# Optimization experiments

Hardware: AMD Instinct MI355X
Metric: run time of the kernel (lower is better)

## Reference

```python
import jax, jax.numpy as jnp
import numpy as np

# Dims: T=out_seq_len, B=batch, D=hidden_dim, H=hidden_dim_de, E=embedding_size, C=feat_channels
T, B, D, H, E, C, FH, FW = 32, 16, 512, 512, 512, 512, 8, 32


def _lstm_dir(x_seq, W_ih, W_hh, b_ih, b_hh, reverse):
    # x_seq: (T, B, D); PyTorch gate order i, f, g, o
    gx = jnp.einsum('tbd,gd->tbg', x_seq, W_ih) + b_ih  # (T, B, 4H)
    Hh = W_hh.shape[1]
    def step(carry, g_t):
        h, c = carry
        g = g_t + h @ W_hh.T + b_hh
        i, f, gg, o = jnp.split(g, 4, axis=-1)
        c = jax.nn.sigmoid(f) * c + jax.nn.sigmoid(i) * jnp.tanh(gg)
        h = jax.nn.sigmoid(o) * jnp.tanh(c)
        return (h, c), h
    init = (jnp.zeros((x_seq.shape[1], Hh), x_seq.dtype),
            jnp.zeros((x_seq.shape[1], Hh), x_seq.dtype))
    _, hs = jax.lax.scan(step, init, gx, reverse=reverse)
    return hs  # (T, B, H)


def setup_inputs() -> dict:
    key = jax.random.key(0)
    ks = jax.random.split(key, 16)
    s = 0.02
    inp = {
        'hidden_en': jax.random.normal(ks[0], (T, B, D), jnp.float32),
        'conv_f': jax.random.normal(ks[1], (B, C, FH, FW), jnp.float32),
        # bidirectional LSTM params (PyTorch layout: W_ih (4H, D), W_hh (4H, H))
        'W_ih_f': jax.random.normal(ks[2], (4 * H, D), jnp.float32) * s,
        'W_hh_f': jax.random.normal(ks[3], (4 * H, H), jnp.float32) * s,
        'b_ih_f': jnp.zeros((4 * H,), jnp.float32),
        'b_hh_f': jnp.zeros((4 * H,), jnp.float32),
        'W_ih_b': jax.random.normal(ks[4], (4 * H, D), jnp.float32) * s,
        'W_hh_b': jax.random.normal(ks[5], (4 * H, H), jnp.float32) * s,
        'b_ih_b': jnp.zeros((4 * H,), jnp.float32),
        'b_hh_b': jnp.zeros((4 * H,), jnp.float32),
        # linear_decode: (H, 2H)
        'W_dec': jax.random.normal(ks[6], (H, 2 * H), jnp.float32) * s,
        'b_dec': jnp.zeros((H,), jnp.float32),
        # conv_em: 3x3, C -> E (OIHW)
        'W_em': jax.random.normal(ks[7], (E, C, 3, 3), jnp.float32) * s,
        'b_em': jnp.zeros((E,), jnp.float32),
        # attention h_em: 1x1 conv == linear H -> E
        'W_hem': jax.random.normal(ks[8], (E, H), jnp.float32) * s,
        'b_hem': jnp.zeros((E,), jnp.float32),
        # conv_att: 1x1 conv E -> 1
        'w_att': jax.random.normal(ks[9], (E,), jnp.float32) * s,
        'b_att': jnp.zeros((), jnp.float32),
    }
    return inp


def reference(hidden_en, conv_f, W_ih_f, W_hh_f, b_ih_f, b_hh_f,
              W_ih_b, W_hh_b, b_ih_b, b_hh_b, W_dec, b_dec,
              W_em, b_em, W_hem, b_hem, w_att, b_att):
    # decoder_ctc: bidirectional LSTM + linear
    h_fwd = _lstm_dir(hidden_en, W_ih_f, W_hh_f, b_ih_f, b_hh_f, reverse=False)
    h_bwd = _lstm_dir(hidden_en, W_ih_b, W_hh_b, b_ih_b, b_hh_b, reverse=True)
    hidden_de = jnp.concatenate([h_fwd, h_bwd], axis=-1) @ W_dec.T + b_dec  # (T, B, H)

    # conv_em: 3x3 same-padding conv, NCHW
    x_em = jax.lax.conv_general_dilated(
        conv_f, W_em, window_strides=(1, 1), padding='SAME',
        dimension_numbers=('NCHW', 'OIHW', 'NCHW')) + b_em[None, :, None, None]  # (B,E,FH,FW)
    att_x_em = jnp.transpose(x_em.reshape(x_em.shape[0], E, -1), (0, 2, 1))  # (B, HW, E)

    # batched attention over all timesteps (dropout is identity at eval)
    h_em = jnp.einsum('tbh,eh->tbe', hidden_de, W_hem) + b_hem  # (T, B, E)
    feat = jnp.tanh(x_em[None] + h_em[:, :, :, None, None])     # (T, B, E, FH, FW)
    scores = jnp.einsum('tbehw,e->tbhw', feat, w_att) + b_att   # (T, B, FH, FW)
    alpha = jax.nn.softmax(scores.reshape(scores.shape[0], scores.shape[1], -1), axis=-1)  # (T,B,HW)
    att = jnp.einsum('tbn,bne->tbe', alpha, att_x_em)           # (T, B, E)

    ctc_out = jnp.concatenate([hidden_de, att], axis=-1)        # (T, B, H+E)
    return jnp.transpose(ctc_out, (1, 0, 2))                    # (B, T, H+E)
```

## Files before the change

### kernel.cpp

```cpp
#include <hip/hip_runtime.h>
#include <hip/hip_bf16.h>
#include <math.h>

#define T_LEN 32
#define BATCH 16
#define DDIM  512
#define HDIM  512
#define EDIM  512
#define CDIM  512
#define FHH   8
#define FWW   32
#define HW    256
#define G4    2048
#define PADH  10
#define PADW  34
#define WLP   520

typedef __attribute__((ext_vector_type(8))) short bf16x8;
typedef __attribute__((ext_vector_type(4))) float f32x4;

__device__ __forceinline__ ushort bfr(float x) {
    union { float f; uint32_t u; } c; c.f = x;
    uint32_t r = (c.u + 0x7FFFu + ((c.u >> 16) & 1u)) >> 16;
    return (ushort)r;
}

__device__ __forceinline__ float frcp(float x) { return __builtin_amdgcn_rcpf(x); }
__device__ __forceinline__ float ftanh(float x) {
    return 1.f - 2.f * frcp(1.f + __expf(2.f * x));
}
__device__ __forceinline__ float fsig(float x) {
    return frcp(1.f + __expf(-x));
}

__device__ __forceinline__ void ld_lds16(const void* g, void* l) {
    __builtin_amdgcn_global_load_lds((const __attribute__((address_space(1))) void*)g,
                                     (__attribute__((address_space(3))) void*)l, 16, 0, 0);
}

__device__ __forceinline__ void st_u16_sc1(ushort* p, ushort v) {
    asm volatile("global_store_short %0, %1, off sc1" :: "v"(p), "v"((uint)v) : "memory");
}
__device__ __forceinline__ void st_i32_sc1(int* p, int v) {
    asm volatile("global_store_dword %0, %1, off sc1" :: "v"(p), "v"(v) : "memory");
}
__device__ __forceinline__ void st_f32_sc1(float* p, float v) {
    asm volatile("global_store_dword %0, %1, off sc1" :: "v"(p), "v"(v) : "memory");
}
__device__ __forceinline__ int ld_i32_sc1(const int* p) {
    int v;
    asm volatile("global_load_dword %0, %1, off sc1\n\ts_waitcnt vmcnt(0)"
                 : "=v"(v) : "v"(p) : "memory");
    return v;
}

struct PrepArgs { const float* s[7]; ushort* d[7]; };
__global__ __launch_bounds__(256) void prep_all(
    PrepArgs a, int* __restrict__ syncbuf,
    const float* __restrict__ conv_f, ushort* __restrict__ padT,
    const float* __restrict__ W_em, ushort* __restrict__ Wt)
{
    __shared__ float tile[32][33];
    const int bid = blockIdx.x, tid = threadIdx.x;
    if (bid < 5120) {
        int i = bid * 256 + tid;
        if (i < 80) st_i32_sc1(syncbuf + i, 0);
        const int e0 = 65536, e1 = 327680, e2 = 589824, e3 = 851968,
                  e4 = 1114112, e5 = 1245184;
        int seg, base;
        if      (i < e0) { seg = 0; base = 0;  }
        else if (i < e1) { seg = 1; base = e0; }
        else if (i < e2) { seg = 2; base = e1; }
        else if (i < e3) { seg = 3; base = e2; }
        else if (i < e4) { seg = 4; base = e3; }
        else if (i < e5) { seg = 5; base = e4; }
        else             { seg = 6; base = e5; }
        int li = i - base;
        float4 v = ((const float4*)a.s[seg])[li];
        ushort4 o;
        o.x = bfr(v.x); o.y = bfr(v.y); o.z = bfr(v.z); o.w = bfr(v.w);
        ((ushort4*)a.d[seg])[li] = o;
        return;
    }
    if (bid < 7168) {
        int id = bid - 5120;
        int s0 = (id & 7) * 32, c0 = ((id >> 3) & 15) * 32, b = id >> 7;
        int lo = tid & 31, hi = tid >> 5;
#pragma unroll
        for (int it = 0; it < 4; ++it) {
            int cl = hi + it * 8;
            tile[cl][lo] = conv_f[((size_t)(b * CDIM + c0 + cl)) * HW + s0 + lo];
        }
        __syncthreads();
#pragma unroll
        for (int it = 0; it < 4; ++it) {
            int sl = hi + it * 8;
            int s = s0 + sl;
            int y = s >> 5, x = s & 31;
            padT[(((size_t)b * PADH + y + 1) * PADW + (x + 1)) * CDIM + c0 + lo] =
                bfr(tile[lo][sl]);
        }
        return;
    }
    if (bid < 7840) {
        int gid = (bid - 7168) * 256 + tid;
        int c4 = gid & 127;
        int cellb = gid >> 7;
        int cell = cellb % 84;
        int b = cellb / 84;
        int y, x;
        if (cell < 34) { y = 0; x = cell; }
        else if (cell < 68) { y = 9; x = cell - 34; }
        else { int k2 = cell - 68; y = 1 + (k2 >> 1); x = (k2 & 1) ? 33 : 0; }
        ((ushort4*)padT)[(((size_t)b * PADH + y) * PADW + x) * (CDIM / 4) + c4] =
            make_ushort4(0, 0, 0, 0);
        return;
    }
    {
        int gid = (bid - 7840) * 256 + tid;
        int c = gid % CDIM;
        int t = gid / CDIM;
        int e = t % EDIM;
        int tap = t / EDIM;
        int dy = tap / 3, dx = tap % 3;
        Wt[gid] = bfr(W_em[((e * CDIM + c) * 3 + dy) * 3 + dx]);
    }
}

__device__ __forceinline__ void tile64_compute(
    const ushort* Ap0, const ushort* Bp0, int K,
    ushort* smem, int tid, f32x4 (&acc)[2][2])
{
    ushort* As = smem;
    ushort* Bs = smem + 2048;
    const int w = tid >> 6, lane = tid & 63;
    ushort* AsW = &As[w * 512];
    ushort* BsW = &Bs[w * 512];
    const int wm = (w >> 1) * 32, wn = (w & 1) * 32;
    const int kb = (lane >> 4) * 8, fr = lane & 15;
    for (int kk = 0; kk < K; kk += 32) {
        __syncthreads();
        ld_lds16(Ap0 + kk, AsW);
        ld_lds16(Bp0 + kk, BsW);
        __syncthreads();
        bf16x8 af[2], bg[2];
#pragma unroll
        for (int i = 0; i < 2; ++i)
            af[i] = *(const bf16x8*)&As[(wm + i * 16 + fr) * 32 + kb];
#pragma unroll
        for (int j = 0; j < 2; ++j)
            bg[j] = *(const bf16x8*)&Bs[(wn + j * 16 + fr) * 32 + kb];
#pragma unroll
        for (int i = 0; i < 2; ++i)
#pragma unroll
            for (int j = 0; j < 2; ++j)
                acc[i][j] = __builtin_amdgcn_mfma_f32_16x16x32_bf16(af[i], bg[j], acc[i][j], 0, 0, 0);
    }
}

__global__ __launch_bounds__(256) void gemm64(
    const ushort* __restrict__ A, const ushort* __restrict__ B,
    const float* __restrict__ bias0,
    float* __restrict__ C, ushort* __restrict__ Cbf, float* __restrict__ Cscat,
    int M, int N, int K)
{
    __shared__ ushort smem[4096];
    const int n0 = blockIdx.x * 64, m0 = blockIdx.y * 64;
    const int tid = threadIdx.x, w = tid >> 6, lane = tid & 63;
    const int r0 = tid >> 2, c0 = (tid & 3) * 8;
    f32x4 acc[2][2];
#pragma unroll
    for (int i = 0; i < 2; ++i)
#pragma unroll
        for (int j = 0; j < 2; ++j) acc[i][j] = {0.f, 0.f, 0.f, 0.f};
    tile64_compute(A + (size_t)(m0 + r0) * K + c0, B + (size_t)(n0 + r0) * K + c0,
                   K, smem, tid, acc);
    const int wm = (w >> 1) * 32, wn = (w & 1) * 32;
    const int col = lane & 15, rq = (lane >> 4) * 4;
#pragma unroll
    for (int i = 0; i < 2; ++i) {
#pragma unroll
        for (int r = 0; r < 4; ++r) {
            int m = m0 + wm + i * 16 + rq + r;
#pragma unroll
            for (int j = 0; j < 2; ++j) {
                int n = n0 + wn + j * 16 + col;
                float v = acc[i][j][r];
                if (bias0) v += bias0[n];
                if (C)   C[(size_t)m * N + n] = v;
                if (Cbf) Cbf[(size_t)m * N + n] = bfr(v);
                if (Cscat) {
                    int t = m >> 4, b = m & 15;
                    Cscat[((size_t)(b * T_LEN + t)) * 1024 + n] = v;
                }
            }
        }
    }
}

__global__ __launch_bounds__(256) void fused_main(
    const ushort* __restrict__ Whh_f, const ushort* __restrict__ Whh_b,
    float* __restrict__ gx_f, float* __restrict__ gx_b,
    const ushort* __restrict__ hen_bf,
    const ushort* __restrict__ Wih_f, const ushort* __restrict__ Wih_b,
    const float* __restrict__ b_ih_f, const float* __restrict__ b_hh_f,
    const float* __restrict__ b_ih_b, const float* __restrict__ b_hh_b,
    ushort* __restrict__ hs_bf,
    int* __restrict__ syncbuf,
    const ushort* __restrict__ padT, const ushort* __restrict__ Wt,
    const float* __restrict__ bias_em, float* __restrict__ xem)
{
    __shared__ ushort smem[64 * WLP];
    const int bid = blockIdx.x, tid = threadIdx.x;
    const int w = tid >> 6, lane = tid & 63;
    int* flags = syncbuf;
    int* gcnt  = syncbuf + 64;

    if (bid < 64) {
        const int dir = bid >> 5;
        const int j0 = (bid & 31) * 16;
        const ushort* W = dir ? Whh_b : Whh_f;
        const float* gx = dir ? gx_b : gx_f;
#pragma unroll
        for (int i = 0; i < 16; ++i) {
            int row = w * 16 + i;
            int g = row >> 4, jl = row & 15;
            bf16x8 v = *(const bf16x8*)(W + ((size_t)(g * 512 + j0 + jl)) * 512 + lane * 8);
            *(bf16x8*)&smem[row * WLP + lane * 8] = v;
        }
        __syncthreads();
        if (tid >= 64) return;
        __builtin_amdgcn_s_setprio(1);

        const int fr = lane & 15, kq = lane >> 4;
        const int j = j0 + fr;
        const int* fq = &flags[dir * 32 + (lane & 31)];
        f32x4 cr = {0.f, 0.f, 0.f, 0.f};
        int mt_done = -1;
        for (int step = 0; step < T_LEN; ++step) {
            const int tcur = dir ? (T_LEN - 1 - step) : step;
            const int mt = tcur >> 2;
            if (mt != mt_done) {
                const int* gp = &gcnt[dir * 8 + mt];
                for (;;) {
                    int v = ld_i32_sc1(gp);
                    if (v >= 32) break;
                    __builtin_amdgcn_s_sleep(4);
                }
                mt_done = mt;
            }
            float gxv[4][4];
#pragma unroll
            for (int r = 0; r < 4; ++r) {
                const float* gxr = gx + ((size_t)tcur * BATCH + (kq * 4 + r)) * G4 + j;
#pragma unroll
                for (int g = 0; g < 4; ++g)
                    asm volatile("global_load_dword %0, %1, off sc1"
                                 : "=v"(gxv[r][g]) : "v"(gxr + g * 512));
            }
            f32x4 acc[4];
#pragma unroll
            for (int g = 0; g < 4; ++g) acc[g] = {0.f, 0.f, 0.f, 0.f};
            if (step > 0) {
                const int tprev = dir ? tcur + 1 : tcur - 1;
                const ushort* hp = hs_bf + ((size_t)tprev * BATCH + fr) * 1024 + dir * 512 + kq * 8;
                bf16x8 hreg[16];
#pragma unroll
                for (int u = 0; u < 16; ++u)
                    asm volatile("global_load_dwordx4 %0, %1, off sc1"
                                 : "=v"(hreg[u]) : "v"(hp + u * 32));
                asm volatile("s_waitcnt vmcnt(0)" ::: "memory");
                __builtin_amdgcn_sched_barrier(0);
#pragma unroll
                for (int u = 0; u < 16; ++u) {
#pragma unroll
                    for (int g = 0; g < 4; ++g) {
                        bf16x8 bb = *(const bf16x8*)&smem[(g * 16 + fr) * WLP + kq * 8 + u * 32];
                        acc[g] = __builtin_amdgcn_mfma_f32_16x16x32_bf16(hreg[u], bb, acc[g], 0, 0, 0);
                    }
                }
            } else {
                asm volatile("s_waitcnt vmcnt(0)" ::: "memory");
                __builtin_amdgcn_sched_barrier(0);
            }
#pragma unroll
            for (int r = 0; r < 4; ++r) {
                int b = kq * 4 + r;
                float gi = gxv[r][0] + acc[0][r];
                float gf = gxv[r][1] + acc[1][r];
                float gg = gxv[r][2] + acc[2][r];
                float go = gxv[r][3] + acc[3][r];
                float si = fsig(gi), sf = fsig(gf), so = fsig(go);
                float c = sf * cr[r] + si * ftanh(gg);
                cr[r] = c;
                float h = so * ftanh(c);
                st_u16_sc1(hs_bf + ((size_t)tcur * BATCH + b) * 1024 + dir * 512 + j, bfr(h));
            }
            if (step < T_LEN - 1) {
                asm volatile("s_waitcnt vmcnt(0)" ::: "memory");
                if (lane == 0) st_i32_sc1(&flags[bid], step + 1);
                const int need = step + 1;
                for (;;) {
                    int v = ld_i32_sc1(fq);
                    if (__all(v >= need)) break;
                    __builtin_amdgcn_s_sleep(1);
                }
            }
        }
        return;
    }

    if (bid < 576) {
        const int gi = bid - 64;
        const int dir = gi & 1;
        const int q = gi >> 1;
        const int nt = q & 31;
        const int mt0 = q >> 5;
        const int mtile = dir ? (7 - mt0) : mt0;
        const ushort* Bw = dir ? Wih_b : Wih_f;
        const float* bi0 = dir ? b_ih_b : b_ih_f;
        const float* bi1 = dir ? b_hh_b : b_hh_f;
        float* Cg = dir ? gx_b : gx_f;
        const int m0 = mtile * 64, n0 = nt * 64;
        const int r0 = tid >> 2, c0 = (tid & 3) * 8;
        f32x4 acc[2][2];
#pragma unroll
        for (int i = 0; i < 2; ++i)
#pragma unroll
            for (int j = 0; j < 2; ++j) acc[i][j] = {0.f, 0.f, 0.f, 0.f};
        tile64_compute(hen_bf + (size_t)(m0 + r0) * 512 + c0,
                       Bw + (size_t)(n0 + r0) * 512 + c0, 512, smem, tid, acc);
        const int wm = (w >> 1) * 32, wn = (w & 1) * 32;
        const int col = lane & 15, rq = (lane >> 4) * 4;
#pragma unroll
        for (int i = 0; i < 2; ++i)
#pragma unroll
            for (int r = 0; r < 4; ++r) {
                int m = m0 + wm + i * 16 + rq + r;
#pragma unroll
                for (int j2 = 0; j2 < 2; ++j2) {
                    int n = n0 + wn + j2 * 16 + col;
                    st_f32_sc1(&Cg[(size_t)m * G4 + n], acc[i][j2][r] + bi0[n] + bi1[n]);
                }
            }
        asm volatile("s_waitcnt vmcnt(0)" ::: "memory");
        __syncthreads();
        if (tid == 0) atomicAdd(&gcnt[dir * 8 + mtile], 1);
        return;
    }

    {
        const int cbid = bid - 576;
        const int n0 = (cbid & 7) * 64, m0 = (cbid >> 3) * 64;
        const int r0 = tid >> 2, c0 = (tid & 3) * 8;
        const int b = m0 >> 8, s0 = m0 & 255, y0 = s0 >> 5;
        const int y = y0 + (r0 >> 5), x = r0 & 31;
        const ushort* Abase = padT + (((size_t)b * PADH + y) * PADW + x) * CDIM + c0;
        const ushort* Bbase = Wt + (size_t)(n0 + r0) * CDIM + c0;
        f32x4 acc[2][2];
#pragma unroll
        for (int i = 0; i < 2; ++i)
#pragma unroll
            for (int j = 0; j < 2; ++j) acc[i][j] = {0.f, 0.f, 0.f, 0.f};
        for (int tap = 0; tap < 9; ++tap) {
            const int dy = tap / 3, dx = tap % 3;
            tile64_compute(Abase + ((size_t)dy * PADW + dx) * CDIM,
                           Bbase + (size_t)tap * EDIM * CDIM, 512, smem, tid, acc);
        }
        const int wm = (w >> 1) * 32, wn = (w & 1) * 32;
        const int col = lane & 15, rq = (lane >> 4) * 4;
#pragma unroll
        for (int i = 0; i < 2; ++i)
#pragma unroll
            for (int r = 0; r < 4; ++r) {
                int m = m0 + wm + i * 16 + rq + r;
                int s = m & 255;
#pragma unroll
                for (int j2 = 0; j2 < 2; ++j2) {
                    int e = n0 + wn + j2 * 16 + col;
                    xem[((size_t)b * EDIM + e) * HW + s] = acc[i][j2][r] + bias_em[e];
                }
            }
    }
}

__global__ __launch_bounds__(256) void attention(
    const float* __restrict__ xem,
    const float* __restrict__ hem,
    const float* __restrict__ watt,
    float* __restrict__ out) {
    int i = blockIdx.x;
    int k = i >> 3;
    int b = ((i & 7) << 1) | (k & 1);
    int t = k >> 1;
    int tb = t * 16 + b;
    int tid = threadIdx.x;
    __shared__ float hl[512], wl[512], al[256], red[8];
    for (int q = tid; q < 512; q += 256) { hl[q] = hem[(size_t)tb * 512 + q]; wl[q] = watt[q]; }
    __syncthreads();
    const float* xb = xem + (size_t)b * EDIM * HW;
    float sc = 0.f;
#pragma unroll 4
    for (int e = 0; e < 512; ++e)
        sc += ftanh(xb[(size_t)e * HW + tid] + hl[e]) * wl[e];
    float m = sc;
#pragma unroll
    for (int o = 32; o; o >>= 1) m = fmaxf(m, __shfl_xor(m, o));
    if ((tid & 63) == 0) red[tid >> 6] = m;
    __syncthreads();
    m = fmaxf(fmaxf(red[0], red[1]), fmaxf(red[2], red[3]));
    float ex = __expf(sc - m);
    float s = ex;
#pragma unroll
    for (int o = 32; o; o >>= 1) s += __shfl_xor(s, o);
    if ((tid & 63) == 0) red[4 + (tid >> 6)] = s;
    __syncthreads();
    s = red[4] + red[5] + red[6] + red[7];
    al[tid] = ex * frcp(s);
    __syncthreads();
    float* ob = out + ((size_t)(b * T_LEN + t)) * 1024 + 512;
    for (int eo = 0; eo < 512; eo += 256) {
        int e = eo + tid;
        const float* xr = xb + (size_t)e * HW;
        float acc = 0.f;
#pragma unroll 4
        for (int n = 0; n < 256; n += 4) {
            float4 v = *(const float4*)&xr[n];
            acc += al[n] * v.x + al[n + 1] * v.y + al[n + 2] * v.z + al[n + 3] * v.w;
        }
        ob[e] = acc;
    }
}

extern "C" void kernel_launch(void* const* d_in, const int* in_sizes, int n_in,
                              void* d_out, int out_size, void* d_ws, size_t ws_size,
                              hipStream_t stream) {
    const float* hidden_en = (const float*)d_in[0];
    const float* conv_f    = (const float*)d_in[1];
    const float* W_ih_f    = (const float*)d_in[2];
    const float* W_hh_f    = (const float*)d_in[3];
    const float* b_ih_f    = (const float*)d_in[4];
    const float* b_hh_f    = (const float*)d_in[5];
    const float* W_ih_b    = (const float*)d_in[6];
    const float* W_hh_b    = (const float*)d_in[7];
    const float* b_ih_b    = (const float*)d_in[8];
    const float* b_hh_b    = (const float*)d_in[9];
    const float* W_dec     = (const float*)d_in[10];
    const float* b_dec     = (const float*)d_in[11];
    const float* W_em      = (const float*)d_in[12];
    const float* b_em      = (const float*)d_in[13];
    const float* W_hem     = (const float*)d_in[14];
    const float* b_hem     = (const float*)d_in[15];
    const float* w_att     = (const float*)d_in[16];
    float* out = (float*)d_out;

    char* p = (char*)d_ws;
    auto alloc = [&](size_t bytes) { void* r = p; p += (bytes + 255) & ~(size_t)255; return r; };
    float*    gx_f    = (float*)alloc((size_t)T_LEN * BATCH * G4 * 4);
    float*    gx_b    = (float*)alloc((size_t)T_LEN * BATCH * G4 * 4);
    float*    h_em    = (float*)alloc((size_t)T_LEN * BATCH * 512 * 4);
    float*    x_em    = (float*)alloc((size_t)BATCH * EDIM * HW * 4);
    ushort*   padT    = (ushort*)alloc((size_t)BATCH * PADH * PADW * CDIM * 2);
    ushort*   Wt      = (ushort*)alloc((size_t)9 * EDIM * CDIM * 2);
    ushort*   hen_bf  = (ushort*)alloc((size_t)T_LEN * BATCH * DDIM * 2);
    ushort*   Wihf_bf = (ushort*)alloc((size_t)G4 * DDIM * 2);
    ushort*   Wihb_bf = (ushort*)alloc((size_t)G4 * DDIM * 2);
    ushort*   Whhf_bf = (ushort*)alloc((size_t)G4 * HDIM * 2);
    ushort*   Whhb_bf = (ushort*)alloc((size_t)G4 * HDIM * 2);
    ushort*   Wdec_bf = (ushort*)alloc((size_t)HDIM * 1024 * 2);
    ushort*   Whem_bf = (ushort*)alloc((size_t)EDIM * HDIM * 2);
    ushort*   hs_bf   = (ushort*)alloc((size_t)T_LEN * BATCH * 1024 * 2);
    ushort*   hde_bf  = (ushort*)alloc((size_t)T_LEN * BATCH * 512 * 2);
    int*      syncbuf = (int*)alloc(512);

    PrepArgs pa;
    pa.s[0] = hidden_en; pa.d[0] = hen_bf;
    pa.s[1] = W_ih_f;    pa.d[1] = Wihf_bf;
    pa.s[2] = W_ih_b;    pa.d[2] = Wihb_bf;
    pa.s[3] = W_hh_f;    pa.d[3] = Whhf_bf;
    pa.s[4] = W_hh_b;    pa.d[4] = Whhb_bf;
    pa.s[5] = W_dec;     pa.d[5] = Wdec_bf;
    pa.s[6] = W_hem;     pa.d[6] = Whem_bf;
    prep_all<<<17056, 256, 0, stream>>>(pa, syncbuf, conv_f, padT, W_em, Wt);

    fused_main<<<1088, 256, 0, stream>>>(Whhf_bf, Whhb_bf, gx_f, gx_b, hen_bf,
                                         Wihf_bf, Wihb_bf, b_ih_f, b_hh_f,
                                         b_ih_b, b_hh_b, hs_bf, syncbuf,
                                         padT, Wt, b_em, x_em);

    gemm64<<<dim3(8, 8), 256, 0, stream>>>(hs_bf, Wdec_bf, b_dec,
                                           nullptr, hde_bf, out, 512, 512, 1024);

    gemm64<<<dim3(8, 8), 256, 0, stream>>>(hde_bf, Whem_bf, b_hem,
                                           h_em, nullptr, nullptr, 512, 512, 512);

    attention<<<512, 256, 0, stream>>>(x_em, h_em, w_att, out);
}
```

Baseline: 253.1 us.

## Fold decode and h_em weights, split LSTM into separate persistent kernel

Precomputes a combined weight W_hem·W_dec and a combined bias so h_em is computed straight from the LSTM hidden states, which removes the serial decode→h_em GEMM dependency. The attention and both output GEMMs move into one tail kernel that synchronises per tile through counters. The conv, input-projection and weight-combination GEMMs run in a worker kernel ahead of the LSTM, so the LSTM no longer waits on flags or overlaps with them. The gx buffer is interleaved by gate so each LSTM step needs one float4 load per row. In exchange, the LSTM recurrence can no longer overlap with the conv GEMM, there is an extra launch, and the combined weight is rounded to bf16 once more.

```diff
diff --git a/kernel.cpp b/kernel.cpp
--- a/kernel.cpp
+++ b/kernel.cpp
@@ -53,12 +53,21 @@
                  : "=v"(v) : "v"(p) : "memory");
     return v;
 }
+__device__ __forceinline__ float ld_f32_sc1(const float* p) {
+    float v;
+    asm volatile("global_load_dword %0, %1, off sc1\n\ts_waitcnt vmcnt(0)"
+                 : "=v"(v) : "v"(p) : "memory");
+    return v;
+}
 
 struct PrepArgs { const float* s[7]; ushort* d[7]; };
 __global__ __launch_bounds__(256) void prep_all(
     PrepArgs a, int* __restrict__ syncbuf,
     const float* __restrict__ conv_f, ushort* __restrict__ padT,
-    const float* __restrict__ W_em, ushort* __restrict__ Wt)
+    const float* __restrict__ W_em, ushort* __restrict__ Wt,
+    const float* __restrict__ W_dec, ushort* __restrict__ WdecT,
+    const float* __restrict__ W_hem, const float* __restrict__ b_dec,
+    const float* __restrict__ b_hem, float* __restrict__ b_comb)
 {
     __shared__ float tile[32][33];
     const int bid = blockIdx.x, tid = threadIdx.x;
@@ -116,7 +125,7 @@
             make_ushort4(0, 0, 0, 0);
         return;
     }
-    {
+    if (bid < 17056) {
         int gid = (bid - 7840) * 256 + tid;
         int c = gid % CDIM;
         int t = gid / CDIM;
@@ -124,6 +133,32 @@
         int tap = t / EDIM;
         int dy = tap / 3, dx = tap % 3;
         Wt[gid] = bfr(W_em[((e * CDIM + c) * 3 + dy) * 3 + dx]);
+        return;
+    }
+    if (bid < 17568) {
+        int idx = bid - 17056;
+        int ht = idx & 15, kt = idx >> 4;
+        int h0 = ht * 32, k0 = kt * 32;
+        int lo = tid & 31, hi = tid >> 5;
+#pragma unroll
+        for (int it = 0; it < 4; ++it) {
+            int i = hi + it * 8;
+            tile[i][lo] = W_dec[(size_t)(h0 + i) * 1024 + k0 + lo];
+        }
+        __syncthreads();
+#pragma unroll
+        for (int it = 0; it < 4; ++it) {
+            int i = hi + it * 8;
+            WdecT[(size_t)(k0 + i) * 512 + h0 + lo] = bfr(tile[lo][i]);
+        }
+        return;
+    }
+    {
+        int e = (bid - 17568) * 256 + tid;
+        float s = b_hem[e];
+        const float* wr = W_hem + (size_t)e * 512;
+        for (int h = 0; h < 512; ++h) s += wr[h] * b_dec[h];
+        b_comb[e] = s;
     }
 }
 
@@ -158,217 +193,40 @@
     }
 }
 
-__global__ __launch_bounds__(256) void gemm64(
-    const ushort* __restrict__ A, const ushort* __restrict__ B,
-    const float* __restrict__ bias0,
-    float* __restrict__ C, ushort* __restrict__ Cbf, float* __restrict__ Cscat,
-    int M, int N, int K)
-{
-    __shared__ ushort smem[4096];
-    const int n0 = blockIdx.x * 64, m0 = blockIdx.y * 64;
-    const int tid = threadIdx.x, w = tid >> 6, lane = tid & 63;
-    const int r0 = tid >> 2, c0 = (tid & 3) * 8;
-    f32x4 acc[2][2];
-#pragma unroll
-    for (int i = 0; i < 2; ++i)
-#pragma unroll
-        for (int j = 0; j < 2; ++j) acc[i][j] = {0.f, 0.f, 0.f, 0.f};
-    tile64_compute(A + (size_t)(m0 + r0) * K + c0, B + (size_t)(n0 + r0) * K + c0,
-                   K, smem, tid, acc);
-    const int wm = (w >> 1) * 32, wn = (w & 1) * 32;
-    const int col = lane & 15, rq = (lane >> 4) * 4;
-#pragma unroll
-    for (int i = 0; i < 2; ++i) {
-#pragma unroll
-        for (int r = 0; r < 4; ++r) {
-            int m = m0 + wm + i * 16 + rq + r;
-#pragma unroll
-            for (int j = 0; j < 2; ++j) {
-                int n = n0 + wn + j * 16 + col;
-                float v = acc[i][j][r];
-                if (bias0) v += bias0[n];
-                if (C)   C[(size_t)m * N + n] = v;
-                if (Cbf) Cbf[(size_t)m * N + n] = bfr(v);
-                if (Cscat) {
-                    int t = m >> 4, b = m & 15;
-                    Cscat[((size_t)(b * T_LEN + t)) * 1024 + n] = v;
-                }
-            }
-        }
-    }
-}
-
-__global__ __launch_bounds__(256) void fused_main(
-    const ushort* __restrict__ Whh_f, const ushort* __restrict__ Whh_b,
-    float* __restrict__ gx_f, float* __restrict__ gx_b,
+__global__ __launch_bounds__(256) void workers(
+    const ushort* __restrict__ padT, const ushort* __restrict__ Wt,
+    const float* __restrict__ bias_em, float* __restrict__ xem,
     const ushort* __restrict__ hen_bf,
     const ushort* __restrict__ Wih_f, const ushort* __restrict__ Wih_b,
     const float* __restrict__ b_ih_f, const float* __restrict__ b_hh_f,
     const float* __restrict__ b_ih_b, const float* __restrict__ b_hh_b,
-    ushort* __restrict__ hs_bf,
-    int* __restrict__ syncbuf,
-    const ushort* __restrict__ padT, const ushort* __restrict__ Wt,
-    const float* __restrict__ bias_em, float* __restrict__ xem)
+    float* __restrict__ gxT_f, float* __restrict__ gxT_b,
+    const ushort* __restrict__ Whem_bf, const ushort* __restrict__ WdecT_bf,
+    ushort* __restrict__ Wcomb_bf)
 {
-    __shared__ ushort smem[64 * WLP];
+    __shared__ ushort smem[4096];
     const int bid = blockIdx.x, tid = threadIdx.x;
     const int w = tid >> 6, lane = tid & 63;
-    int* flags = syncbuf;
-    int* gcnt  = syncbuf + 64;
-
-    if (bid < 64) {
-        const int dir = bid >> 5;
-        const int j0 = (bid & 31) * 16;
-        const ushort* W = dir ? Whh_b : Whh_f;
-        const float* gx = dir ? gx_b : gx_f;
-#pragma unroll
-        for (int i = 0; i < 16; ++i) {
-            int row = w * 16 + i;
-            int g = row >> 4, jl = row & 15;
-            bf16x8 v = *(const bf16x8*)(W + ((size_t)(g * 512 + j0 + jl)) * 512 + lane * 8);
-            *(bf16x8*)&smem[row * WLP + lane * 8] = v;
-        }
-        __syncthreads();
-        if (tid >= 64) return;
-        __builtin_amdgcn_s_setprio(1);
-
-        const int fr = lane & 15, kq = lane >> 4;
-        const int j = j0 + fr;
-        const int* fq = &flags[dir * 32 + (lane & 31)];
-        f32x4 cr = {0.f, 0.f, 0.f, 0.f};
-        int mt_done = -1;
-        for (int step = 0; step < T_LEN; ++step) {
-            const int tcur = dir ? (T_LEN - 1 - step) : step;
-            const int mt = tcur >> 2;
-            if (mt != mt_done) {
-                const int* gp = &gcnt[dir * 8 + mt];
-                for (;;) {
-                    int v = ld_i32_sc1(gp);
-                    if (v >= 32) break;
-                    __builtin_amdgcn_s_sleep(4);
-                }
-                mt_done = mt;
-            }
-            float gxv[4][4];
-#pragma unroll
-            for (int r = 0; r < 4; ++r) {
-                const float* gxr = gx + ((size_t)tcur * BATCH + (kq * 4 + r)) * G4 + j;
-#pragma unroll
-                for (int g = 0; g < 4; ++g)
-                    asm volatile("global_load_dword %0, %1, off sc1"
-                                 : "=v"(gxv[r][g]) : "v"(gxr + g * 512));
-            }
-            f32x4 acc[4];
-#pragma unroll
-            for (int g = 0; g < 4; ++g) acc[g] = {0.f, 0.f, 0.f, 0.f};
-            if (step > 0) {
-                const int tprev = dir ? tcur + 1 : tcur - 1;
-                const ushort* hp = hs_bf + ((size_t)tprev * BATCH + fr) * 1024 + dir * 512 + kq * 8;
-                bf16x8 hreg[16];
-#pragma unroll
-                for (int u = 0; u < 16; ++u)
-                    asm volatile("global_load_dwordx4 %0, %1, off sc1"
-                                 : "=v"(hreg[u]) : "v"(hp + u * 32));
-                asm volatile("s_waitcnt vmcnt(0)" ::: "memory");
-                __builtin_amdgcn_sched_barrier(0);
-#pragma unroll
-                for (int u = 0; u < 16; ++u) {
-#pragma unroll
-                    for (int g = 0; g < 4; ++g) {
-                        bf16x8 bb = *(const bf16x8*)&smem[(g * 16 + fr) * WLP + kq * 8 + u * 32];
-                        acc[g] = __builtin_amdgcn_mfma_f32_16x16x32_bf16(hreg[u], bb, acc[g], 0, 0, 0);
-                    }
-                }
-            } else {
-                asm volatile("s_waitcnt vmcnt(0)" ::: "memory");
-                __builtin_amdgcn_sched_barrier(0);
-            }
-#pragma unroll
-            for (int r = 0; r < 4; ++r) {
-                int b = kq * 4 + r;
-                float gi = gxv[r][0] + acc[0][r];
-                float gf = gxv[r][1] + acc[1][r];
-                float gg = gxv[r][2] + acc[2][r];
-                float go = gxv[r][3] + acc[3][r];
-                float si = fsig(gi), sf = fsig(gf), so = fsig(go);
-                float c = sf * cr[r] + si * ftanh(gg);
-                cr[r] = c;
-                float h = so * ftanh(c);
-                st_u16_sc1(hs_bf + ((size_t)tcur * BATCH + b) * 1024 + dir * 512 + j, bfr(h));
-            }
-            if (step < T_LEN - 1) {
-                asm volatile("s_waitcnt vmcnt(0)" ::: "memory");
-                if (lane == 0) st_i32_sc1(&flags[bid], step + 1);
-                const int need = step + 1;
-                for (;;) {
-                    int v = ld_i32_sc1(fq);
-                    if (__all(v >= need)) break;
-                    __builtin_amdgcn_s_sleep(1);
-                }
-            }
-        }
-        return;
-    }
-
-    if (bid < 576) {
-        const int gi = bid - 64;
-        const int dir = gi & 1;
-        const int q = gi >> 1;
-        const int nt = q & 31;
-        const int mt0 = q >> 5;
-        const int mtile = dir ? (7 - mt0) : mt0;
-        const ushort* Bw = dir ? Wih_b : Wih_f;
-        const float* bi0 = dir ? b_ih_b : b_ih_f;
-        const float* bi1 = dir ? b_hh_b : b_hh_f;
-        float* Cg = dir ? gx_b : gx_f;
-        const int m0 = mtile * 64, n0 = nt * 64;
-        const int r0 = tid >> 2, c0 = (tid & 3) * 8;
-        f32x4 acc[2][2];
-#pragma unroll
-        for (int i = 0; i < 2; ++i)
-#pragma unroll
-            for (int j = 0; j < 2; ++j) acc[i][j] = {0.f, 0.f, 0.f, 0.f};
-        tile64_compute(hen_bf + (size_t)(m0 + r0) * 512 + c0,
-                       Bw + (size_t)(n0 + r0) * 512 + c0, 512, smem, tid, acc);
-        const int wm = (w >> 1) * 32, wn = (w & 1) * 32;
-        const int col = lane & 15, rq = (lane >> 4) * 4;
-#pragma unroll
-        for (int i = 0; i < 2; ++i)
-#pragma unroll
-            for (int r = 0; r < 4; ++r) {
-                int m = m0 + wm + i * 16 + rq + r;
-#pragma unroll
-                for (int j2 = 0; j2 < 2; ++j2) {
-                    int n = n0 + wn + j2 * 16 + col;
-                    st_f32_sc1(&Cg[(size_t)m * G4 + n], acc[i][j2][r] + bi0[n] + bi1[n]);
-                }
-            }
-        asm volatile("s_waitcnt vmcnt(0)" ::: "memory");
-        __syncthreads();
-        if (tid == 0) atomicAdd(&gcnt[dir * 8 + mtile], 1);
-        return;
-    }
-
-    {
-        const int cbid = bid - 576;
-        const int n0 = (cbid & 7) * 64, m0 = (cbid >> 3) * 64;
-        const int r0 = tid >> 2, c0 = (tid & 3) * 8;
+    const int r0 = tid >> 2, c0 = (tid & 3) * 8;
+    const int wm = (w >> 1) * 32, wn = (w & 1) * 32;
+    const int col = lane & 15, rq = (lane >> 4) * 4;
+    f32x4 acc[2][2];
+#pragma unroll
+    for (int i = 0; i < 2; ++i)
+#pragma unroll
+        for (int j = 0; j < 2; ++j) acc[i][j] = {0.f, 0.f, 0.f, 0.f};
+
+    if (bid < 512) {
+        const int n0 = (bid & 7) * 64, m0 = (bid >> 3) * 64;
         const int b = m0 >> 8, s0 = m0 & 255, y0 = s0 >> 5;
         const int y = y0 + (r0 >> 5), x = r0 & 31;
         const ushort* Abase = padT + (((size_t)b * PADH + y) * PADW + x) * CDIM + c0;
         const ushort* Bbase = Wt + (size_t)(n0 + r0) * CDIM + c0;
-        f32x4 acc[2][2];
-#pragma unroll
-        for (int i = 0; i < 2; ++i)
-#pragma unroll
-            for (int j = 0; j < 2; ++j) acc[i][j] = {0.f, 0.f, 0.f, 0.f};
         for (int tap = 0; tap < 9; ++tap) {
             const int dy = tap / 3, dx = tap % 3;
             tile64_compute(Abase + ((size_t)dy * PADW + dx) * CDIM,
                            Bbase + (size_t)tap * EDIM * CDIM, 512, smem, tid, acc);
         }
-        const int wm = (w >> 1) * 32, wn = (w & 1) * 32;
-        const int col = lane & 15, rq = (lane >> 4) * 4;
 #pragma unroll
         for (int i = 0; i < 2; ++i)
 #pragma unroll
@@ -381,54 +239,251 @@
                     xem[((size_t)b * EDIM + e) * HW + s] = acc[i][j2][r] + bias_em[e];
                 }
             }
-    }
-}
-
-__global__ __launch_bounds__(256) void attention(
-    const float* __restrict__ xem,
-    const float* __restrict__ hem,
-    const float* __restrict__ watt,
-    float* __restrict__ out) {
-    int i = blockIdx.x;
-    int k = i >> 3;
-    int b = ((i & 7) << 1) | (k & 1);
-    int t = k >> 1;
-    int tb = t * 16 + b;
-    int tid = threadIdx.x;
-    __shared__ float hl[512], wl[512], al[256], red[8];
-    for (int q = tid; q < 512; q += 256) { hl[q] = hem[(size_t)tb * 512 + q]; wl[q] = watt[q]; }
+        return;
+    }
+    if (bid < 1024) {
+        const int gi = bid - 512;
+        const int dir = gi & 1;
+        const int q = gi >> 1;
+        const int mt = q >> 5, nt = q & 31;
+        const ushort* Bw = dir ? Wih_b : Wih_f;
+        const float* bi0 = dir ? b_ih_b : b_ih_f;
+        const float* bi1 = dir ? b_hh_b : b_hh_f;
+        float* Cg = dir ? gxT_b : gxT_f;
+        const int m0 = mt * 64, n0 = nt * 64;
+        tile64_compute(hen_bf + (size_t)(m0 + r0) * 512 + c0,
+                       Bw + (size_t)(n0 + r0) * 512 + c0, 512, smem, tid, acc);
+#pragma unroll
+        for (int i = 0; i < 2; ++i)
+#pragma unroll
+            for (int r = 0; r < 4; ++r) {
+                int m = m0 + wm + i * 16 + rq + r;
+#pragma unroll
+                for (int j2 = 0; j2 < 2; ++j2) {
+                    int n = n0 + wn + j2 * 16 + col;
+                    Cg[(size_t)m * G4 + (n & 511) * 4 + (n >> 9)] =
+                        acc[i][j2][r] + bi0[n] + bi1[n];
+                }
+            }
+        return;
+    }
+    {
+        const int wb = bid - 1024;
+        const int mt = wb >> 4, nt = wb & 15;
+        const int m0 = mt * 64, n0 = nt * 64;
+        tile64_compute(Whem_bf + (size_t)(m0 + r0) * 512 + c0,
+                       WdecT_bf + (size_t)(n0 + r0) * 512 + c0, 512, smem, tid, acc);
+#pragma unroll
+        for (int i = 0; i < 2; ++i)
+#pragma unroll
+            for (int r = 0; r < 4; ++r) {
+                int m = m0 + wm + i * 16 + rq + r;
+#pragma unroll
+                for (int j2 = 0; j2 < 2; ++j2) {
+                    int n = n0 + wn + j2 * 16 + col;
+                    Wcomb_bf[(size_t)m * 1024 + n] = bfr(acc[i][j2][r]);
+                }
+            }
+    }
+}
+
+__global__ __launch_bounds__(256) void lstm_persist(
+    const ushort* __restrict__ Whh_f, const ushort* __restrict__ Whh_b,
+    const float* __restrict__ gxT_f, const float* __restrict__ gxT_b,
+    ushort* __restrict__ hs_bf, int* __restrict__ flags)
+{
+    __shared__ ushort smem[64 * WLP];
+    const int bid = blockIdx.x, tid = threadIdx.x;
+    const int w = tid >> 6, lane = tid & 63;
+    const int dir = bid >> 5;
+    const int j0 = (bid & 31) * 16;
+    const ushort* W = dir ? Whh_b : Whh_f;
+    const float* gx = dir ? gxT_b : gxT_f;
+#pragma unroll
+    for (int i = 0; i < 16; ++i) {
+        int row = w * 16 + i;
+        int g = row >> 4, jl = row & 15;
+        bf16x8 v = *(const bf16x8*)(W + ((size_t)(g * 512 + j0 + jl)) * 512 + lane * 8);
+        *(bf16x8*)&smem[row * WLP + lane * 8] = v;
+    }
     __syncthreads();
-    const float* xb = xem + (size_t)b * EDIM * HW;
-    float sc = 0.f;
+    if (tid >= 64) return;
+    __builtin_amdgcn_s_setprio(1);
+
+    const int fr = lane & 15, kq = lane >> 4;
+    const int j = j0 + fr;
+    const int* fq = &flags[dir * 32 + (lane & 31)];
+    f32x4 cr = {0.f, 0.f, 0.f, 0.f};
+    for (int step = 0; step < T_LEN; ++step) {
+        const int tcur = dir ? (T_LEN - 1 - step) : step;
+        float4 gq[4];
+#pragma unroll
+        for (int r = 0; r < 4; ++r)
+            gq[r] = *(const float4*)(gx + (((size_t)tcur * BATCH + kq * 4 + r) * 512 + j) * 4);
+        f32x4 acc[4];
+#pragma unroll
+        for (int g = 0; g < 4; ++g) acc[g] = {0.f, 0.f, 0.f, 0.f};
+        if (step > 0) {
+            const int tprev = dir ? tcur + 1 : tcur - 1;
+            const ushort* hp = hs_bf + ((size_t)tprev * BATCH + fr) * 1024 + dir * 512 + kq * 8;
+            bf16x8 hreg[16];
+#pragma unroll
+            for (int u = 0; u < 16; ++u)
+                asm volatile("global_load_dwordx4 %0, %1, off sc1"
+                             : "=v"(hreg[u]) : "v"(hp + u * 32));
+            asm volatile("s_waitcnt vmcnt(0)" ::: "memory");
+            __builtin_amdgcn_sched_barrier(0);
+#pragma unroll
+            for (int u = 0; u < 16; ++u) {
+#pragma unroll
+                for (int g = 0; g < 4; ++g) {
+                    bf16x8 bb = *(const bf16x8*)&smem[(g * 16 + fr) * WLP + kq * 8 + u * 32];
+                    acc[g] = __builtin_amdgcn_mfma_f32_16x16x32_bf16(hreg[u], bb, acc[g], 0, 0, 0);
+                }
+            }
+        }
+#pragma unroll
+        for (int r = 0; r < 4; ++r) {
+            int b = kq * 4 + r;
+            float gi = gq[r].x + acc[0][r];
+            float gf = gq[r].y + acc[1][r];
+            float gg = gq[r].z + acc[2][r];
+            float go = gq[r].w + acc[3][r];
+            float si = fsig(gi), sf = fsig(gf), so = fsig(go);
+            float c = sf * cr[r] + si * ftanh(gg);
+            cr[r] = c;
+            float h = so * ftanh(c);
+            st_u16_sc1(hs_bf + ((size_t)tcur * BATCH + b) * 1024 + dir * 512 + j, bfr(h));
+        }
+        if (step < T_LEN - 1) {
+            asm volatile("s_waitcnt vmcnt(0)" ::: "memory");
+            if (lane == 0) st_i32_sc1(&flags[bid], step + 1);
+            const int need = step + 1;
+            for (;;) {
+                int v = ld_i32_sc1(fq);
+                if (__all(v >= need)) break;
+                __builtin_amdgcn_s_sleep(1);
+            }
+        }
+    }
+}
+
+__global__ __launch_bounds__(256) void tail(
+    const ushort* __restrict__ hs_bf, const ushort* __restrict__ Wdec_bf,
+    const float* __restrict__ b_dec, float* __restrict__ out,
+    const ushort* __restrict__ Wcomb_bf, const float* __restrict__ b_comb,
+    float* __restrict__ h_em,
+    const float* __restrict__ xem, const float* __restrict__ watt,
+    int* __restrict__ syncbuf)
+{
+    __shared__ ushort smem[4096];
+    int* hcnt = syncbuf + 64;
+    const int bid = blockIdx.x, tid = threadIdx.x;
+    const int w = tid >> 6, lane = tid & 63;
+    const int r0 = tid >> 2, c0 = (tid & 3) * 8;
+    const int wm = (w >> 1) * 32, wn = (w & 1) * 32;
+    const int col = lane & 15, rq = (lane >> 4) * 4;
+
+    if (bid < 128) {
+        f32x4 acc[2][2];
+#pragma unroll
+        for (int i = 0; i < 2; ++i)
+#pragma unroll
+            for (int j = 0; j < 2; ++j) acc[i][j] = {0.f, 0.f, 0.f, 0.f};
+        if (bid < 64) {
+            const int mt = bid >> 3, nt = bid & 7;
+            const int m0 = mt * 64, n0 = nt * 64;
+            tile64_compute(hs_bf + (size_t)(m0 + r0) * 1024 + c0,
+                           Wdec_bf + (size_t)(n0 + r0) * 1024 + c0, 1024, smem, tid, acc);
+#pragma unroll
+            for (int i = 0; i < 2; ++i)
+#pragma unroll
+                for (int r = 0; r < 4; ++r) {
+                    int m = m0 + wm + i * 16 + rq + r;
+                    int t = m >> 4, b = m & 15;
+#pragma unroll
+                    for (int j2 = 0; j2 < 2; ++j2) {
+                        int n = n0 + wn + j2 * 16 + col;
+                        out[((size_t)(b * T_LEN + t)) * 1024 + n] = acc[i][j2][r] + b_dec[n];
+                    }
+                }
+        } else {
+            const int blk = bid - 64;
+            const int mt = blk >> 3, nt = blk & 7;
+            const int m0 = mt * 64, n0 = nt * 64;
+            tile64_compute(hs_bf + (size_t)(m0 + r0) * 1024 + c0,
+                           Wcomb_bf + (size_t)(n0 + r0) * 1024 + c0, 1024, smem, tid, acc);
+#pragma unroll
+            for (int i = 0; i < 2; ++i)
+#pragma unroll
+                for (int r = 0; r < 4; ++r) {
+                    int m = m0 + wm + i * 16 + rq + r;
+#pragma unroll
+                    for (int j2 = 0; j2 < 2; ++j2) {
+                        int n = n0 + wn + j2 * 16 + col;
+                        st_f32_sc1(&h_em[(size_t)m * 512 + n], acc[i][j2][r] + b_comb[n]);
+                    }
+                }
+            asm volatile("s_waitcnt vmcnt(0)" ::: "memory");
+            __syncthreads();
+            if (tid == 0) atomicAdd(&hcnt[mt], 1);
+        }
+        return;
+    }
+
+    {
+        int i = bid - 128;
+        int k = i >> 3;
+        int b = ((i & 7) << 1) | (k & 1);
+        int t = k >> 1;
+        int tb = t * 16 + b;
+        const int mt = tb >> 6;
+        if (tid == 0) {
+            while (ld_i32_sc1(&hcnt[mt]) < 8) __builtin_amdgcn_s_sleep(8);
+        }
+        __syncthreads();
+        float* fs = (float*)smem;
+        float* hl = fs;
+        float* wl = fs + 512;
+        float* al = fs + 1024;
+        float* red = fs + 1280;
+        for (int q = tid; q < 512; q += 256) {
+            hl[q] = ld_f32_sc1(&h_em[(size_t)tb * 512 + q]);
+            wl[q] = watt[q];
+        }
+        __syncthreads();
+        const float* xb = xem + (size_t)b * EDIM * HW;
+        float sc = 0.f;
 #pragma unroll 4
-    for (int e = 0; e < 512; ++e)
-        sc += ftanh(xb[(size_t)e * HW + tid] + hl[e]) * wl[e];
-    float m = sc;
-#pragma unroll
-    for (int o = 32; o; o >>= 1) m = fmaxf(m, __shfl_xor(m, o));
-    if ((tid & 63) == 0) red[tid >> 6] = m;
-    __syncthreads();
-    m = fmaxf(fmaxf(red[0], red[1]), fmaxf(red[2], red[3]));
-    float ex = __expf(sc - m);
-    float s = ex;
-#pragma unroll
-    for (int o = 32; o; o >>= 1) s += __shfl_xor(s, o);
-    if ((tid & 63) == 0) red[4 + (tid >> 6)] = s;
-    __syncthreads();
-    s = red[4] + red[5] + red[6] + red[7];
-    al[tid] = ex * frcp(s);
-    __syncthreads();
-    float* ob = out + ((size_t)(b * T_LEN + t)) * 1024 + 512;
-    for (int eo = 0; eo < 512; eo += 256) {
-        int e = eo + tid;
-        const float* xr = xb + (size_t)e * HW;
-        float acc = 0.f;
+        for (int e = 0; e < 512; ++e)
+            sc += ftanh(xb[(size_t)e * HW + tid] + hl[e]) * wl[e];
+        float m = sc;
+#pragma unroll
+        for (int o = 32; o; o >>= 1) m = fmaxf(m, __shfl_xor(m, o));
+        if ((tid & 63) == 0) red[tid >> 6] = m;
+        __syncthreads();
+        m = fmaxf(fmaxf(red[0], red[1]), fmaxf(red[2], red[3]));
+        float ex = __expf(sc - m);
+        float s = ex;
+#pragma unroll
+        for (int o = 32; o; o >>= 1) s += __shfl_xor(s, o);
+        if ((tid & 63) == 0) red[4 + (tid >> 6)] = s;
+        __syncthreads();
+        s = red[4] + red[5] + red[6] + red[7];
+        al[tid] = ex * frcp(s);
+        __syncthreads();
+        float* ob = out + ((size_t)(b * T_LEN + t)) * 1024 + 512;
+        for (int eo = 0; eo < 512; eo += 256) {
+            int e = eo + tid;
+            const float* xr = xb + (size_t)e * HW;
+            float acc2 = 0.f;
 #pragma unroll 4
-        for (int n = 0; n < 256; n += 4) {
-            float4 v = *(const float4*)&xr[n];
-            acc += al[n] * v.x + al[n + 1] * v.y + al[n + 2] * v.z + al[n + 3] * v.w;
-        }
-        ob[e] = acc;
+            for (int n = 0; n < 256; n += 4) {
+                float4 v = *(const float4*)&xr[n];
+                acc2 += al[n] * v.x + al[n + 1] * v.y + al[n + 2] * v.z + al[n + 3] * v.w;
+            }
+            ob[e] = acc2;
+        }
     }
 }
 
@@ -456,8 +511,8 @@
 
     char* p = (char*)d_ws;
     auto alloc = [&](size_t bytes) { void* r = p; p += (bytes + 255) & ~(size_t)255; return r; };
-    float*    gx_f    = (float*)alloc((size_t)T_LEN * BATCH * G4 * 4);
-    float*    gx_b    = (float*)alloc((size_t)T_LEN * BATCH * G4 * 4);
+    float*    gxT_f   = (float*)alloc((size_t)T_LEN * BATCH * G4 * 4);
+    float*    gxT_b   = (float*)alloc((size_t)T_LEN * BATCH * G4 * 4);
     float*    h_em    = (float*)alloc((size_t)T_LEN * BATCH * 512 * 4);
     float*    x_em    = (float*)alloc((size_t)BATCH * EDIM * HW * 4);
     ushort*   padT    = (ushort*)alloc((size_t)BATCH * PADH * PADW * CDIM * 2);
@@ -469,8 +524,10 @@
     ushort*   Whhb_bf = (ushort*)alloc((size_t)G4 * HDIM * 2);
     ushort*   Wdec_bf = (ushort*)alloc((size_t)HDIM * 1024 * 2);
     ushort*   Whem_bf = (ushort*)alloc((size_t)EDIM * HDIM * 2);
+    ushort*   WdecT_bf= (ushort*)alloc((size_t)1024 * 512 * 2);
+    ushort*   Wcomb_bf= (ushort*)alloc((size_t)512 * 1024 * 2);
+    float*    b_comb  = (float*)alloc(512 * 4);
     ushort*   hs_bf   = (ushort*)alloc((size_t)T_LEN * BATCH * 1024 * 2);
-    ushort*   hde_bf  = (ushort*)alloc((size_t)T_LEN * BATCH * 512 * 2);
     int*      syncbuf = (int*)alloc(512);
 
     PrepArgs pa;
@@ -481,18 +538,17 @@
     pa.s[4] = W_hh_b;    pa.d[4] = Whhb_bf;
     pa.s[5] = W_dec;     pa.d[5] = Wdec_bf;
     pa.s[6] = W_hem;     pa.d[6] = Whem_bf;
-    prep_all<<<17056, 256, 0, stream>>>(pa, syncbuf, conv_f, padT, W_em, Wt);
-
-    fused_main<<<1088, 256, 0, stream>>>(Whhf_bf, Whhb_bf, gx_f, gx_b, hen_bf,
-                                         Wihf_bf, Wihb_bf, b_ih_f, b_hh_f,
-                                         b_ih_b, b_hh_b, hs_bf, syncbuf,
-                                         padT, Wt, b_em, x_em);
-
-    gemm64<<<dim3(8, 8), 256, 0, stream>>>(hs_bf, Wdec_bf, b_dec,
-                                           nullptr, hde_bf, out, 512, 512, 1024);
-
-    gemm64<<<dim3(8, 8), 256, 0, stream>>>(hde_bf, Whem_bf, b_hem,
-                                           h_em, nullptr, nullptr, 512, 512, 512);
-
-    attention<<<512, 256, 0, stream>>>(x_em, h_em, w_att, out);
-}
+    prep_all<<<17570, 256, 0, stream>>>(pa, syncbuf, conv_f, padT, W_em, Wt,
+                                        W_dec, WdecT_bf, W_hem, b_dec, b_hem, b_comb);
+
+    workers<<<1152, 256, 0, stream>>>(padT, Wt, b_em, x_em, hen_bf,
+                                      Wihf_bf, Wihb_bf, b_ih_f, b_hh_f,
+                                      b_ih_b, b_hh_b, gxT_f, gxT_b,
+                                      Whem_bf, WdecT_bf, Wcomb_bf);
+
+    lstm_persist<<<64, 256, 0, stream>>>(Whhf_bf, Whhb_bf, gxT_f, gxT_b,
+                                         hs_bf, syncbuf);
+
+    tail<<<640, 256, 0, stream>>>(hs_bf, Wdec_bf, b_dec, out,
+                                  Wcomb_bf, b_comb, h_em, x_em, w_att, syncbuf);
+}
```

Result: slower. 287.4 us (+13.5%).
